# Kernel tuning notes

Hardware: AMD Instinct MI355X
Metric: run time of the kernel (lower is better)

The kernel has to match this reference:

```python
import jax, jax.numpy as jnp
import numpy as np

N_HEADS = 8
D_EMBED = 512
D_HEAD = D_EMBED // N_HEADS


def setup_inputs() -> dict:
    key = jax.random.key(0)
    ks = jax.random.split(key, 5)
    B, S, D = 8, 2048, D_EMBED
    scale_in = 1.0 / np.sqrt(D)
    x = jax.random.normal(ks[0], (B, S, D), dtype=jnp.float32)
    # torch nn.Linear weights: (out_features, in_features)
    w_in = jax.random.normal(ks[1], (3 * D, D), dtype=jnp.float32) * scale_in
    b_in = jax.random.normal(ks[2], (3 * D,), dtype=jnp.float32) * scale_in
    w_out = jax.random.normal(ks[3], (D, D), dtype=jnp.float32) * scale_in
    b_out = jax.random.normal(ks[4], (D,), dtype=jnp.float32) * scale_in
    return {"x": x, "w_in": w_in, "b_in": b_in, "w_out": w_out, "b_out": b_out}


def reference(x, w_in, b_in, w_out, b_out):
    B, S, D = x.shape
    H, Dh = N_HEADS, D_HEAD
    # fused QKV projection (torch Linear: x @ W^T + b)
    qkv = x @ w_in.T + b_in                     # (B, S, 3D)
    q, k, v = jnp.split(qkv, 3, axis=-1)        # each (B, S, D)
    # split heads -> (B, H, S, Dh)
    def heads(t):
        return t.reshape(B, S, H, Dh).transpose(0, 2, 1, 3)
    q, k, v = heads(q), heads(k), heads(v)
    # scaled dot-product attention (full matrix, as in source)
    scores = jnp.einsum("bhqd,bhkd->bhqk", q, k) / jnp.sqrt(jnp.float32(Dh))
    weights = jax.nn.softmax(scores, axis=-1)   # (B, H, S, S)
    out = jnp.einsum("bhqk,bhkd->bhqd", weights, v)
    out = out.transpose(0, 2, 1, 3).reshape(B, S, D)
    return out @ w_out.T + b_out
```

## Files before the change

kernel.cpp:

```cpp
#include <hip/hip_runtime.h>
#include <stdint.h>

#define SEQ   2048
#define DEMB  512
#define NH    8
#define DH    64
#define BATCH 8
#define M_ROWS (BATCH * SEQ)
#define QKLD  1024
#define QSCALE 0.18033688011112042f

typedef __attribute__((ext_vector_type(8))) __bf16 bf16x8;
typedef __attribute__((ext_vector_type(4))) __bf16 bf16x4;
typedef __attribute__((ext_vector_type(4))) float  f32x4;
typedef __attribute__((ext_vector_type(8))) uint16_t u16x8;
typedef __attribute__((ext_vector_type(4))) uint32_t u32x4;

__device__ __forceinline__ void gll16(const __bf16* g, __bf16* l) {
    __builtin_amdgcn_global_load_lds(
        (__attribute__((address_space(1))) void*)(__bf16*)g,
        (__attribute__((address_space(3))) void*)l, 16, 0, 0);
}

__device__ __forceinline__ bf16x8 ld8(const __bf16* p) {
    return *(const bf16x8*)p;
}

__device__ __forceinline__ uint32_t pkpair(float a, float b) {
    const uint16_t lo = __builtin_bit_cast(uint16_t, (__bf16)a);
    const uint16_t hi = __builtin_bit_cast(uint16_t, (__bf16)b);
    return (uint32_t)lo | ((uint32_t)hi << 16);
}

__device__ __forceinline__ int sw(int row, int chunk) {
    return row * 64 + ((chunk ^ (row & 7)) << 3);
}

__device__ __forceinline__ void stage_gll_sw(const __bf16* g, int gld,
                                             __bf16* l, int wave, int lane) {
    const int lr = lane >> 3;
    const int scol = ((lane & 7) ^ lr) * 8;
    #pragma unroll
    for (int i = 0; i < 2; i++) {
        const int r0 = i * 32 + wave * 8;
        gll16(g + (size_t)(r0 + lr) * gld + scol, l + r0 * 64);
    }
}

__device__ __forceinline__ void stage_gll(const __bf16* src, __bf16* dst,
                                          int ld, int wave, int lane) {
    const int srow = lane >> 3, scol = (lane & 7) * 8;
    #pragma unroll
    for (int i = 0; i < 4; i++) {
        const int r0 = (i * 4 + wave) * 8;
        gll16(src + (size_t)(r0 + srow) * ld + scol, dst + r0 * 64);
    }
}

#define NXQ (M_ROWS * DEMB / 4)
#define NWQ (3 * DEMB * DEMB / 4)
#define NOQ (DEMB * DEMB / 4)

__global__ __launch_bounds__(256)
void cvt_all(const float* __restrict__ x, const float* __restrict__ w_in,
             __bf16* __restrict__ xb, __bf16* __restrict__ wb) {
    const int i = blockIdx.x * 256 + threadIdx.x;
    const float4* src;
    bf16x4* dst;
    if (i < NXQ) { src = (const float4*)x + i;         dst = (bf16x4*)xb + i; }
    else if (i < NXQ + NWQ) {
        const int j = i - NXQ;
        src = (const float4*)w_in + j;  dst = (bf16x4*)wb + j;
    } else return;
    const float4 v = *src;
    bf16x4 b;
    b[0] = (__bf16)v.x; b[1] = (__bf16)v.y;
    b[2] = (__bf16)v.z; b[3] = (__bf16)v.w;
    *dst = b;
}

__global__ __launch_bounds__(256)
void cvt_wout(const float* __restrict__ w, __bf16* __restrict__ wb) {
    const int i = blockIdx.x * 256 + threadIdx.x;
    if (i < NOQ) {
        const float4 v = ((const float4*)w)[i];
        bf16x4 b;
        b[0] = (__bf16)v.x; b[1] = (__bf16)v.y;
        b[2] = (__bf16)v.z; b[3] = (__bf16)v.w;
        ((bf16x4*)wb)[i] = b;
    }
}

__global__ __launch_bounds__(256)
void gemm_qkv(const __bf16* __restrict__ A, const __bf16* __restrict__ W,
              const float* __restrict__ bias, __bf16* __restrict__ qk,
              __bf16* __restrict__ vt) {
    constexpr int K = DEMB;
    __shared__ __align__(16) __bf16 SM[128 * 128];
    __bf16* As = SM;
    __bf16* Bs = SM + 128 * 64;

    const int tid  = threadIdx.x;
    const int wave = tid >> 6, lane = tid & 63;
    const int quad = lane >> 4, l16 = lane & 15;
    const int m0 = blockIdx.x * 128, n0 = blockIdx.y * 128;
    const int wm = wave & 1, wn = wave >> 1;
    const bool qkblk = (n0 < QKLD);

    f32x4 acc[4][4] = {};

    for (int k0 = 0; k0 < K; k0 += 64) {
        __syncthreads();
        stage_gll(A + (size_t)m0 * K + k0, As, K, wave, lane);
        stage_gll(W + (size_t)n0 * K + k0, Bs, K, wave, lane);
        __syncthreads();
        #pragma unroll
        for (int ks = 0; ks < 2; ks++) {
            bf16x8 af[4], bf[4];
            #pragma unroll
            for (int t = 0; t < 4; t++) {
                af[t] = ld8(&As[(wm * 64 + t * 16 + l16) * 64 + ks * 32 + quad * 8]);
                bf[t] = ld8(&Bs[(wn * 64 + t * 16 + l16) * 64 + ks * 32 + quad * 8]);
            }
            if (qkblk) {
                #pragma unroll
                for (int j = 0; j < 4; j++)
                    #pragma unroll
                    for (int i = 0; i < 4; i++)
                        acc[j][i] = __builtin_amdgcn_mfma_f32_16x16x32_bf16(
                            bf[j], af[i], acc[j][i], 0, 0, 0);
            } else {
                #pragma unroll
                for (int i = 0; i < 4; i++)
                    #pragma unroll
                    for (int j = 0; j < 4; j++)
                        acc[i][j] = __builtin_amdgcn_mfma_f32_16x16x32_bf16(
                            af[i], bf[j], acc[i][j], 0, 0, 0);
            }
        }
    }

    __syncthreads();

    if (qkblk) {
        const float scl = (n0 < DEMB) ? QSCALE : 1.0f;
        #pragma unroll
        for (int j = 0; j < 4; j++) {
            const int nl = wn * 64 + j * 16 + quad * 4;
            const float4 bv4 = *(const float4*)&bias[n0 + nl];
            const int chunk = nl >> 3;
            #pragma unroll
            for (int i = 0; i < 4; i++) {
                const int ml = wm * 64 + i * 16 + l16;
                bf16x4 pk;
                pk[0] = (__bf16)((acc[j][i][0] + bv4.x) * scl);
                pk[1] = (__bf16)((acc[j][i][1] + bv4.y) * scl);
                pk[2] = (__bf16)((acc[j][i][2] + bv4.z) * scl);
                pk[3] = (__bf16)((acc[j][i][3] + bv4.w) * scl);
                const int phys = ((chunk & 7) ^ (ml & 7)) | (chunk & 8);
                *(bf16x4*)(&SM[ml * 128 + phys * 8 + (nl & 7)]) = pk;
            }
        }
        __syncthreads();
        const int g = tid >> 4, li = tid & 15;
        #pragma unroll
        for (int it = 0; it < 8; it++) {
            const int row = it * 16 + g;
            const int phys = ((li & 7) ^ (row & 7)) | (li & 8);
            bf16x8 v = ld8(&SM[row * 128 + phys * 8]);
            *(bf16x8*)(qk + (size_t)(m0 + row) * QKLD + n0 + li * 8) = v;
        }
    } else {
        const int hd0 = n0 - QKLD;
        const int bb = m0 >> 11, s0 = m0 & (SEQ - 1);
        #pragma unroll
        for (int j = 0; j < 4; j++) {
            const int n = n0 + wn * 64 + j * 16 + l16;
            const float bv = bias[n];
            const int hdl = wn * 64 + j * 16 + l16;
            #pragma unroll
            for (int i = 0; i < 4; i++) {
                const int sl = wm * 64 + i * 16 + quad * 4;
                bf16x4 pk;
                #pragma unroll
                for (int r = 0; r < 4; r++)
                    pk[r] = (__bf16)(acc[i][j][r] + bv);
                const int chunk = sl >> 3;
                const int phys = (((chunk & 7) ^ (hdl & 7)) | (chunk & 8));
                *(bf16x4*)(&SM[hdl * 128 + phys * 8 + (sl & 7)]) = pk;
            }
        }
        __syncthreads();
        const int g = tid >> 4, li = tid & 15;
        #pragma unroll
        for (int it = 0; it < 8; it++) {
            const int row = it * 16 + g;
            const int phys = (((li & 7) ^ (row & 7)) | (li & 8));
            bf16x8 v = ld8(&SM[row * 128 + phys * 8]);
            *(bf16x8*)(vt + ((size_t)(bb * DEMB + hd0 + row)) * SEQ + s0 + li * 8) = v;
        }
    }
}

__global__ __launch_bounds__(256, 3)
void attn_flash(const __bf16* __restrict__ qk, const __bf16* __restrict__ vt,
                __bf16* __restrict__ outp) {
    const int qt = blockIdx.x, h = blockIdx.y, b = blockIdx.z;
    const int tid  = threadIdx.x;
    const int wave = tid >> 6, lane = tid & 63;
    const int quad = lane >> 4, l16 = lane & 15;

    __shared__ __align__(16) __bf16 Ks[2][64 * 64];
    __shared__ __align__(16) __bf16 Vt[2][64 * 64];

    const size_t brow = (size_t)b * SEQ;
    const int q0 = qt * 128 + wave * 32;
    const __bf16* kbase = qk + brow * QKLD + DEMB + h * DH;
    const __bf16* vbase = vt + ((size_t)(b * DEMB + h * DH)) * SEQ;

    const u16x8 one16 = {0x3F80, 0x3F80, 0x3F80, 0x3F80,
                         0x3F80, 0x3F80, 0x3F80, 0x3F80};
    const bf16x8 ONES = __builtin_bit_cast(bf16x8, one16);

    bf16x8 qf[2][2];
    #pragma unroll
    for (int qb = 0; qb < 2; qb++) {
        const __bf16* qp = qk + (brow + q0 + qb * 16 + l16) * QKLD + h * DH + quad * 8;
        qf[qb][0] = ld8(qp);
        qf[qb][1] = ld8(qp + 32);
    }

    f32x4 o[2][4] = {};
    f32x4 osum[2] = {};
    f32x4 st[2][4];
    bf16x8 pf[2][2];

    auto do_qk = [&](int tt) {
        const int bufq = tt & 1;
        #pragma unroll
        for (int kt = 0; kt < 4; kt++) {
            bf16x8 kf0 = ld8(&Ks[bufq][sw(kt * 16 + l16, quad)]);
            bf16x8 kf1 = ld8(&Ks[bufq][sw(kt * 16 + l16, 4 + quad)]);
            #pragma unroll
            for (int qb = 0; qb < 2; qb++) {
                f32x4 c = {};
                c = __builtin_amdgcn_mfma_f32_16x16x32_bf16(kf0, qf[qb][0], c, 0, 0, 0);
                c = __builtin_amdgcn_mfma_f32_16x16x32_bf16(kf1, qf[qb][1], c, 0, 0, 0);
                st[qb][kt] = c;
            }
        }
    };

    auto do_softmax = [&]() {
        #pragma unroll
        for (int qb = 0; qb < 2; qb++) {
            uint32_t pk[4][2];
            #pragma unroll
            for (int kt = 0; kt < 4; kt++) {
                pk[kt][0] = pkpair(__builtin_amdgcn_exp2f(st[qb][kt][0]),
                                   __builtin_amdgcn_exp2f(st[qb][kt][1]));
                pk[kt][1] = pkpair(__builtin_amdgcn_exp2f(st[qb][kt][2]),
                                   __builtin_amdgcn_exp2f(st[qb][kt][3]));
            }
            #pragma unroll
            for (int f = 0; f < 2; f++) {
                uint32_t a0 = pk[2 * f][0], b0 = pk[2 * f + 1][0];
                uint32_t a1 = pk[2 * f][1], b1 = pk[2 * f + 1][1];
                {
                    auto r = __builtin_amdgcn_permlane32_swap(a0, b0, false, false);
                    a0 = r[0]; b0 = r[1];
                }
                {
                    auto r = __builtin_amdgcn_permlane32_swap(a1, b1, false, false);
                    a1 = r[0]; b1 = r[1];
                }
                {
                    auto r = __builtin_amdgcn_permlane16_swap(a0, b0, false, false);
                    a0 = r[0]; b0 = r[1];
                }
                {
                    auto r = __builtin_amdgcn_permlane16_swap(a1, b1, false, false);
                    a1 = r[0]; b1 = r[1];
                }
                u32x4 d;
                d[0] = a0; d[1] = a1; d[2] = b0; d[3] = b1;
                pf[qb][f] = __builtin_bit_cast(bf16x8, d);
            }
            osum[qb] = __builtin_amdgcn_mfma_f32_16x16x32_bf16(pf[qb][0], ONES, osum[qb], 0, 0, 0);
            osum[qb] = __builtin_amdgcn_mfma_f32_16x16x32_bf16(pf[qb][1], ONES, osum[qb], 0, 0, 0);
        }
    };

    auto do_pv = [&](int tt) {
        const int bufv = tt & 1;
        #pragma unroll
        for (int db = 0; db < 4; db++) {
            bf16x8 vf0 = ld8(&Vt[bufv][sw(db * 16 + l16, quad)]);
            bf16x8 vf1 = ld8(&Vt[bufv][sw(db * 16 + l16, 4 + quad)]);
            #pragma unroll
            for (int qb = 0; qb < 2; qb++) {
                o[qb][db] = __builtin_amdgcn_mfma_f32_16x16x32_bf16(pf[qb][0], vf0, o[qb][db], 0, 0, 0);
                o[qb][db] = __builtin_amdgcn_mfma_f32_16x16x32_bf16(pf[qb][1], vf1, o[qb][db], 0, 0, 0);
            }
        }
    };

    constexpr int NT = SEQ / 64;

    stage_gll_sw(kbase,                      QKLD, Ks[0], wave, lane);
    stage_gll_sw(vbase,                      SEQ,  Vt[0], wave, lane);
    stage_gll_sw(kbase + (size_t)64 * QKLD,  QKLD, Ks[1], wave, lane);
    __syncthreads();
    do_qk(0);

    for (int t = 0; t < NT - 1; ++t) {
        __syncthreads();
        if (t + 2 < NT)
            stage_gll_sw(kbase + (size_t)(t + 2) * 64 * QKLD, QKLD, Ks[t & 1], wave, lane);
        stage_gll_sw(vbase + (t + 1) * 64, SEQ, Vt[(t + 1) & 1], wave, lane);

        do_softmax();
        __builtin_amdgcn_s_setprio(1);
        do_qk(t + 1);
        do_pv(t);
        __builtin_amdgcn_s_setprio(0);
    }

    __syncthreads();
    do_softmax();
    do_pv(NT - 1);

    #pragma unroll
    for (int qb = 0; qb < 2; qb++)
        #pragma unroll
        for (int r = 0; r < 4; r++) {
            const float linv = __builtin_amdgcn_rcpf(osum[qb][r]);
            const int q = q0 + qb * 16 + quad * 4 + r;
            #pragma unroll
            for (int db = 0; db < 4; db++)
                outp[(brow + q) * DEMB + h * DH + db * 16 + l16] =
                    (__bf16)(o[qb][db][r] * linv);
        }
}

__global__ __launch_bounds__(256)
void gemm_out(const __bf16* __restrict__ A, const __bf16* __restrict__ W,
              const float* __restrict__ bias, float* __restrict__ C,
              int N, int K) {
    __shared__ __align__(16) __bf16 SMO[2 * 128 * 64];
    __bf16* As = SMO;
    __bf16* Bs = SMO + 128 * 64;

    const int tid  = threadIdx.x;
    const int wave = tid >> 6, lane = tid & 63;
    const int quad = lane >> 4, l16 = lane & 15;
    const int m0 = blockIdx.x * 128, n0 = blockIdx.y * 128;
    const int wm = wave & 1, wn = wave >> 1;

    f32x4 acc[4][4] = {};

    for (int k0 = 0; k0 < K; k0 += 64) {
        __syncthreads();
        stage_gll(A + (size_t)m0 * K + k0, As, K, wave, lane);
        stage_gll(W + (size_t)n0 * K + k0, Bs, K, wave, lane);
        __syncthreads();
        #pragma unroll
        for (int ks = 0; ks < 2; ks++) {
            bf16x8 af[4], bf[4];
            #pragma unroll
            for (int t = 0; t < 4; t++) {
                af[t] = ld8(&As[(wm * 64 + t * 16 + l16) * 64 + ks * 32 + quad * 8]);
                bf[t] = ld8(&Bs[(wn * 64 + t * 16 + l16) * 64 + ks * 32 + quad * 8]);
            }
            #pragma unroll
            for (int j = 0; j < 4; j++)
                #pragma unroll
                for (int i = 0; i < 4; i++)
                    acc[j][i] = __builtin_amdgcn_mfma_f32_16x16x32_bf16(
                        bf[j], af[i], acc[j][i], 0, 0, 0);
        }
    }

    __syncthreads();
    float* SMf = (float*)SMO;

    #pragma unroll
    for (int p = 0; p < 2; p++) {
        if (p) __syncthreads();
        if (wm == p) {
            #pragma unroll
            for (int j = 0; j < 4; j++) {
                const int nl = wn * 64 + j * 16 + quad * 4;
                const float4 bv4 = *(const float4*)&bias[n0 + nl];
                const int chunkf = nl >> 2;
                #pragma unroll
                for (int i = 0; i < 4; i++) {
                    const int ml = i * 16 + l16;
                    const int physf = ((chunkf & 7) ^ (ml & 7)) | (chunkf & 24);
                    float4 v;
                    v.x = acc[j][i][0] + bv4.x;
                    v.y = acc[j][i][1] + bv4.y;
                    v.z = acc[j][i][2] + bv4.z;
                    v.w = acc[j][i][3] + bv4.w;
                    *(float4*)(&SMf[ml * 128 + physf * 4]) = v;
                }
            }
        }
        __syncthreads();
        const int g2 = tid >> 5, li2 = tid & 31;
        #pragma unroll
        for (int it = 0; it < 8; it++) {
            const int row = it * 8 + g2;
            const int physf = ((li2 & 7) ^ (row & 7)) | (li2 & 24);
            float4 v = *(const float4*)&SMf[row * 128 + physf * 4];
            *(float4*)(&C[(size_t)(m0 + p * 64 + row) * N + n0 + li2 * 4]) = v;
        }
    }
}

extern "C" void kernel_launch(void* const* d_in, const int* in_sizes, int n_in,
                              void* d_out, int out_size, void* d_ws, size_t ws_size,
                              hipStream_t stream) {
    const float* x     = (const float*)d_in[0];
    const float* w_in  = (const float*)d_in[1];
    const float* b_in  = (const float*)d_in[2];
    const float* w_out = (const float*)d_in[3];
    const float* b_out = (const float*)d_in[4];

    __bf16* qk   = (__bf16*)d_ws;
    __bf16* vtb  = qk + (size_t)M_ROWS * QKLD;
    __bf16* xbuf = vtb + (size_t)BATCH * DEMB * SEQ;
    __bf16* aout = xbuf;
    __bf16* woutb = vtb;
    __bf16* winb = (__bf16*)((char*)d_out + 24u * 1024 * 1024);
    float*  outp = (float*)d_out;

    cvt_all<<<(NXQ + NWQ + 255) / 256, 256, 0, stream>>>(x, w_in, xbuf, winb);
    gemm_qkv<<<dim3(M_ROWS / 128, 12), 256, 0, stream>>>(xbuf, winb, b_in, qk, vtb);
    attn_flash<<<dim3(SEQ / 128, NH, BATCH), 256, 0, stream>>>(qk, vtb, aout);
    cvt_wout<<<NOQ / 256, 256, 0, stream>>>(w_out, woutb);
    gemm_out<<<dim3(M_ROWS / 128, DEMB / 128), 256, 0, stream>>>(
        aout, woutb, b_out, outp, DEMB, DEMB);
}
```

Before: 230.0 us.

## Fuse exp2 into QK step, keep packed bf16 scores, raise occupancy to 4

Applies exp2 and bf16 packing right after the QK MFMAs, so scores are held as packed bf16 pairs instead of fp32 vectors, roughly halving score register usage. The loop now runs PV for the current tile before QK+exp for the next tile, and the launch bound asks for 4 blocks per SIMD instead of 3. This aims to raise occupancy and overlap exp with MFMA work. The tighter register budget risks spills, and the reordering may weaken MFMA/exp interleaving.

New measurement: 231.6 us, median of 2. No clear change (+0.7%).

```diff
diff --git a/kernel.cpp b/kernel.cpp
--- a/kernel.cpp
+++ b/kernel.cpp
@@ -202,7 +202,7 @@
     }
 }
 
-__global__ __launch_bounds__(256, 3)
+__global__ __launch_bounds__(256, 4)
 void attn_flash(const __bf16* __restrict__ qk, const __bf16* __restrict__ vt,
                 __bf16* __restrict__ outp) {
     const int qt = blockIdx.x, h = blockIdx.y, b = blockIdx.z;
@@ -232,10 +232,10 @@
 
     f32x4 o[2][4] = {};
     f32x4 osum[2] = {};
-    f32x4 st[2][4];
+    uint32_t pk[2][4][2];
     bf16x8 pf[2][2];
 
-    auto do_qk = [&](int tt) {
+    auto do_qkexp = [&](int tt) {
         const int bufq = tt & 1;
         #pragma unroll
         for (int kt = 0; kt < 4; kt++) {
@@ -246,26 +246,21 @@
                 f32x4 c = {};
                 c = __builtin_amdgcn_mfma_f32_16x16x32_bf16(kf0, qf[qb][0], c, 0, 0, 0);
                 c = __builtin_amdgcn_mfma_f32_16x16x32_bf16(kf1, qf[qb][1], c, 0, 0, 0);
-                st[qb][kt] = c;
+                pk[qb][kt][0] = pkpair(__builtin_amdgcn_exp2f(c[0]),
+                                       __builtin_amdgcn_exp2f(c[1]));
+                pk[qb][kt][1] = pkpair(__builtin_amdgcn_exp2f(c[2]),
+                                       __builtin_amdgcn_exp2f(c[3]));
             }
         }
     };
 
-    auto do_softmax = [&]() {
+    auto do_permlane_osum = [&]() {
         #pragma unroll
         for (int qb = 0; qb < 2; qb++) {
-            uint32_t pk[4][2];
-            #pragma unroll
-            for (int kt = 0; kt < 4; kt++) {
-                pk[kt][0] = pkpair(__builtin_amdgcn_exp2f(st[qb][kt][0]),
-                                   __builtin_amdgcn_exp2f(st[qb][kt][1]));
-                pk[kt][1] = pkpair(__builtin_amdgcn_exp2f(st[qb][kt][2]),
-                                   __builtin_amdgcn_exp2f(st[qb][kt][3]));
-            }
             #pragma unroll
             for (int f = 0; f < 2; f++) {
-                uint32_t a0 = pk[2 * f][0], b0 = pk[2 * f + 1][0];
-                uint32_t a1 = pk[2 * f][1], b1 = pk[2 * f + 1][1];
+                uint32_t a0 = pk[qb][2 * f][0], b0 = pk[qb][2 * f + 1][0];
+                uint32_t a1 = pk[qb][2 * f][1], b1 = pk[qb][2 * f + 1][1];
                 {
                     auto r = __builtin_amdgcn_permlane32_swap(a0, b0, false, false);
                     a0 = r[0]; b0 = r[1];
@@ -311,7 +306,7 @@
     stage_gll_sw(vbase,                      SEQ,  Vt[0], wave, lane);
     stage_gll_sw(kbase + (size_t)64 * QKLD,  QKLD, Ks[1], wave, lane);
     __syncthreads();
-    do_qk(0);
+    do_qkexp(0);
 
     for (int t = 0; t < NT - 1; ++t) {
         __syncthreads();
@@ -319,15 +314,15 @@
             stage_gll_sw(kbase + (size_t)(t + 2) * 64 * QKLD, QKLD, Ks[t & 1], wave, lane);
         stage_gll_sw(vbase + (t + 1) * 64, SEQ, Vt[(t + 1) & 1], wave, lane);
 
-        do_softmax();
+        do_permlane_osum();
         __builtin_amdgcn_s_setprio(1);
-        do_qk(t + 1);
         do_pv(t);
+        do_qkexp(t + 1);
         __builtin_amdgcn_s_setprio(0);
     }
 
     __syncthreads();
-    do_softmax();
+    do_permlane_osum();
     do_pv(NT - 1);
 
     #pragma unroll
```
